# Optimization experiments

Hardware: AMD Instinct MI355X
Metric: run time of the kernel (lower is better)

## Reference

```python
import jax, jax.numpy as jnp
import numpy as np

N, NQ, M, DQ, DK, DV, H = 4, 512, 512, 256, 256, 256, 256


def setup_inputs() -> dict:
    key = jax.random.key(0)
    ks = jax.random.split(key, 6)
    scale_q = 1.0 / np.sqrt(DQ)
    scale_k = 1.0 / np.sqrt(DK)
    scale_v = 1.0 / np.sqrt(H)
    return {
        "query": jax.random.normal(ks[0], (N, NQ, DQ), jnp.float32),
        "key": jax.random.normal(ks[1], (N, M, DK), jnp.float32),
        "value": jax.random.normal(ks[2], (N, M, DV), jnp.float32),
        "W_q": jax.random.normal(ks[3], (DQ, H), jnp.float32) * scale_q,
        "W_k": jax.random.normal(ks[4], (DK, H), jnp.float32) * scale_k,
        "W_v": jax.random.normal(ks[5], (H,), jnp.float32) * scale_v,
    }


def reference(query, key, value, W_q, W_k, W_v):
    # project: (N, n, H) and (N, m, H)
    q = jnp.einsum("bnd,dh->bnh", query, W_q)
    k = jnp.einsum("bmd,dh->bmh", key, W_k)
    # broadcast add -> (N, n, m, H), tanh, project H->1 -> scores (N, n, m)
    scores = jnp.einsum("bnmh,h->bnm", jnp.tanh(q[:, :, None, :] + k[:, None, :, :]), W_v)
    attn = jax.nn.softmax(scores, axis=-1)  # (N, n, m)
    return jnp.einsum("bnm,bmv->bnv", attn, value)
```

## Files before the change

kernel.cpp:

```cpp
#include <hip/hip_runtime.h>
#include <hip/hip_bf16.h>

#define NB 4
#define NQL 512
#define ML 512
#define DDIM 256
#define HDIM 256

static constexpr float TWO_LOG2E = 2.8853900817779268f;
static constexpr float LOG2E     = 1.4426950408889634f;

__global__ __launch_bounds__(256) void proj_kernel(
    const float* __restrict__ q_src, const float* __restrict__ k_src,
    const float* __restrict__ Wq,    const float* __restrict__ Wk,
    float* __restrict__ EqT,         float* __restrict__ EkT)
{
    const int z = blockIdx.z;
    const int b = z & 3;
    const int which = z >> 2;
    const float* __restrict__ src  = which ? k_src : q_src;
    const float* __restrict__ W    = which ? Wk    : Wq;
    float* __restrict__       outT = which ? EkT   : EqT;

    const int l0 = blockIdx.x * 32;
    const int h0 = blockIdx.y * 64;
    const int t  = threadIdx.x;
    const int tx = t & 15;
    const int ty = t >> 4;

    __shared__ float sX[32][36];
    __shared__ float sW[32][68];

    float acc[2][4];
    #pragma unroll
    for (int i = 0; i < 2; i++)
        #pragma unroll
        for (int j = 0; j < 4; j++) acc[i][j] = 0.f;

    const int llA = t >> 3, dgA = t & 7;
    const int ddB = t >> 3, hgB = t & 7;

    for (int d0 = 0; d0 < DDIM; d0 += 32) {
        float4 xv = *(const float4*)&src[(size_t)(b * NQL + l0 + llA) * DDIM + d0 + dgA * 4];
        const float* wrow = &W[(size_t)(d0 + ddB) * HDIM + h0 + hgB * 8];
        float4 wa = ((const float4*)wrow)[0];
        float4 wb = ((const float4*)wrow)[1];
        __syncthreads();
        sX[dgA * 4 + 0][llA] = xv.x;
        sX[dgA * 4 + 1][llA] = xv.y;
        sX[dgA * 4 + 2][llA] = xv.z;
        sX[dgA * 4 + 3][llA] = xv.w;
        *(float4*)&sW[ddB][hgB * 8]     = wa;
        *(float4*)&sW[ddB][hgB * 8 + 4] = wb;
        __syncthreads();
        #pragma unroll
        for (int dd = 0; dd < 32; dd++) {
            float4 w4 = *(const float4*)&sW[dd][tx * 4];
            float2 x2 = *(const float2*)&sX[dd][ty * 2];
            acc[0][0] = fmaf(x2.x, w4.x, acc[0][0]);
            acc[0][1] = fmaf(x2.x, w4.y, acc[0][1]);
            acc[0][2] = fmaf(x2.x, w4.z, acc[0][2]);
            acc[0][3] = fmaf(x2.x, w4.w, acc[0][3]);
            acc[1][0] = fmaf(x2.y, w4.x, acc[1][0]);
            acc[1][1] = fmaf(x2.y, w4.y, acc[1][1]);
            acc[1][2] = fmaf(x2.y, w4.z, acc[1][2]);
            acc[1][3] = fmaf(x2.y, w4.w, acc[1][3]);
        }
    }

    #pragma unroll
    for (int j = 0; j < 4; j++) {
        float2 o;
        o.x = __builtin_amdgcn_exp2f(acc[0][j] * TWO_LOG2E);
        o.y = __builtin_amdgcn_exp2f(acc[1][j] * TWO_LOG2E);
        *(float2*)&outT[(size_t)(b * HDIM + h0 + tx * 4 + j) * NQL + l0 + ty * 2] = o;
    }
}

__global__ __launch_bounds__(256) void scores_kernel(
    const float* __restrict__ EqT, const float* __restrict__ EkT,
    const float* __restrict__ Wv, float* __restrict__ P,
    float* __restrict__ Spart)
{
    const int b  = blockIdx.z;
    const int mt = blockIdx.x;
    const int m0 = mt * 32;
    const int n0 = blockIdx.y * 32;
    const int t  = threadIdx.x;
    const int tx = t & 15;
    const int ty = t >> 4;

    __shared__ float sQ[32][36];
    __shared__ float sK[32][36];
    __shared__ float sWV[32];

    float acc00 = 0.f, acc01 = 0.f, acc10 = 0.f, acc11 = 0.f;
    float swv = 0.f;

    const int hhA = t >> 3, cgA = t & 7;

    for (int h0 = 0; h0 < HDIM; h0 += 32) {
        float4 qv = *(const float4*)&EqT[(size_t)(b * HDIM + h0 + hhA) * NQL + n0 + cgA * 4];
        float4 kv = *(const float4*)&EkT[(size_t)(b * HDIM + h0 + hhA) * ML  + m0 + cgA * 4];
        float wv_ld = (t < 32) ? Wv[h0 + t] : 0.f;
        __syncthreads();
        *(float4*)&sQ[hhA][cgA * 4] = qv;
        *(float4*)&sK[hhA][cgA * 4] = kv;
        if (t < 32) sWV[t] = wv_ld;
        __syncthreads();
        #pragma unroll 8
        for (int hh = 0; hh < 32; hh++) {
            float2 q2 = *(const float2*)&sQ[hh][ty * 2];
            float2 k2 = *(const float2*)&sK[hh][tx * 2];
            float wv = sWV[hh];
            swv += wv;
            const float nw2 = -2.0f * wv;
            float a00 = fmaf(q2.x, k2.x, 1.0f);
            float a01 = fmaf(q2.x, k2.y, 1.0f);
            float a10 = fmaf(q2.y, k2.x, 1.0f);
            float a11 = fmaf(q2.y, k2.y, 1.0f);
            float r0 = __builtin_amdgcn_rcpf(a00 * a01);
            float r1 = __builtin_amdgcn_rcpf(a10 * a11);
            acc00 = fmaf(nw2, r0 * a01, acc00);
            acc01 = fmaf(nw2, r0 * a00, acc01);
            acc10 = fmaf(nw2, r1 * a11, acc10);
            acc11 = fmaf(nw2, r1 * a10, acc11);
        }
    }

    float2 o0, o1;
    o0.x = __builtin_amdgcn_exp2f((swv + acc00) * LOG2E);
    o0.y = __builtin_amdgcn_exp2f((swv + acc01) * LOG2E);
    o1.x = __builtin_amdgcn_exp2f((swv + acc10) * LOG2E);
    o1.y = __builtin_amdgcn_exp2f((swv + acc11) * LOG2E);
    *(float2*)&P[(size_t)(b * NQL + n0 + ty * 2 + 0) * ML + m0 + tx * 2] = o0;
    *(float2*)&P[(size_t)(b * NQL + n0 + ty * 2 + 1) * ML + m0 + tx * 2] = o1;

    float rs0 = o0.x + o0.y;
    float rs1 = o1.x + o1.y;
    #pragma unroll
    for (int off = 1; off < 16; off <<= 1) {
        rs0 += __shfl_xor(rs0, off);
        rs1 += __shfl_xor(rs1, off);
    }
    if (tx == 0) {
        Spart[(size_t)(mt * NB + b) * NQL + n0 + ty * 2 + 0] = rs0;
        Spart[(size_t)(mt * NB + b) * NQL + n0 + ty * 2 + 1] = rs1;
    }
}

__global__ __launch_bounds__(256) void av_kernel(
    const float* __restrict__ A, const float* __restrict__ Spart,
    const float* __restrict__ V, float* __restrict__ O)
{
    const int b  = blockIdx.z;
    const int v0 = blockIdx.x * 64;
    const int n0 = blockIdx.y * 16;
    const int t  = threadIdx.x;
    const int tx = t & 15;
    const int ty = t >> 4;

    __shared__ float sA[32][20];
    __shared__ float sV[32][68];
    __shared__ float sInv[16];

    if (t < 16) {
        float s = 0.f;
        #pragma unroll
        for (int mt = 0; mt < 16; ++mt)
            s += Spart[(size_t)(mt * NB + b) * NQL + n0 + t];
        sInv[t] = 1.0f / s;
    }

    float4 acc = {0.f, 0.f, 0.f, 0.f};

    const int nnA = t >> 4, mgA = t & 15;
    const int mmB = t >> 3, vgB = t & 7;

    for (int m0 = 0; m0 < ML; m0 += 32) {
        float2 av = *(const float2*)&A[(size_t)(b * NQL + n0 + nnA) * ML + m0 + mgA * 2];
        const float* vrow = &V[(size_t)(b * ML + m0 + mmB) * DDIM + v0 + vgB * 8];
        float4 va = ((const float4*)vrow)[0];
        float4 vb = ((const float4*)vrow)[1];
        __syncthreads();
        sA[mgA * 2 + 0][nnA] = av.x;
        sA[mgA * 2 + 1][nnA] = av.y;
        *(float4*)&sV[mmB][vgB * 8]     = va;
        *(float4*)&sV[mmB][vgB * 8 + 4] = vb;
        __syncthreads();
        #pragma unroll
        for (int mm = 0; mm < 32; mm++) {
            float a = sA[mm][ty];
            float4 v4 = *(const float4*)&sV[mm][tx * 4];
            acc.x = fmaf(a, v4.x, acc.x);
            acc.y = fmaf(a, v4.y, acc.y);
            acc.z = fmaf(a, v4.z, acc.z);
            acc.w = fmaf(a, v4.w, acc.w);
        }
    }

    const float inv = sInv[ty];
    float4 o;
    o.x = acc.x * inv;
    o.y = acc.y * inv;
    o.z = acc.z * inv;
    o.w = acc.w * inv;
    *(float4*)&O[(size_t)(b * NQL + n0 + ty) * DDIM + v0 + tx * 4] = o;
}

extern "C" void kernel_launch(void* const* d_in, const int* in_sizes, int n_in,
                              void* d_out, int out_size, void* d_ws, size_t ws_size,
                              hipStream_t stream)
{
    const float* query = (const float*)d_in[0];
    const float* key   = (const float*)d_in[1];
    const float* value = (const float*)d_in[2];
    const float* Wq    = (const float*)d_in[3];
    const float* Wk    = (const float*)d_in[4];
    const float* Wv    = (const float*)d_in[5];
    float* out = (float*)d_out;

    float* EqT   = (float*)d_ws;
    float* EkT   = EqT + (size_t)NB * HDIM * NQL;
    float* P     = EkT + (size_t)NB * HDIM * ML;
    float* Spart = P + (size_t)NB * NQL * ML;

    dim3 gProj(NQL / 32, HDIM / 64, NB * 2);
    proj_kernel<<<gProj, 256, 0, stream>>>(query, key, Wq, Wk, EqT, EkT);

    dim3 gSc(ML / 32, NQL / 32, NB);
    scores_kernel<<<gSc, 256, 0, stream>>>(EqT, EkT, Wv, P, Spart);

    dim3 gAv(DDIM / 64, NQL / 16, NB);
    av_kernel<<<gAv, 256, 0, stream>>>(P, Spart, value, out);
}
```

Measured before the change: 133.6 us.

## Split AV reduction across wavefronts with register prefetch and 4x4 micro-tiles

Restructures the attention-times-value kernel so each of the four wavefronts handles a separate quarter of the m dimension. Each thread now computes a 4x4 register tile instead of 1x4, and the partial sums are combined through shared memory at the end. The next chunk of A and V is loaded into registers while the current chunk is computed, which overlaps global loads with FMAs and cuts the number of loop iterations and barriers. The cost is more shared memory, more registers per thread and an extra reduction step.

```diff
diff --git a/kernel.cpp b/kernel.cpp
--- a/kernel.cpp
+++ b/kernel.cpp
@@ -157,11 +157,14 @@
     const int v0 = blockIdx.x * 64;
     const int n0 = blockIdx.y * 16;
     const int t  = threadIdx.x;
-    const int tx = t & 15;
-    const int ty = t >> 4;
-
-    __shared__ float sA[32][20];
-    __shared__ float sV[32][68];
+    const int lane = t & 63;
+    const int w    = t >> 6;
+    const int tx   = lane & 15;
+    const int tn   = lane >> 4;
+
+    __shared__ float sA[4][32][20];
+    __shared__ float sV[4][32][68];
+    __shared__ float sRed[3][16][64];
     __shared__ float sInv[16];
 
     if (t < 16) {
@@ -172,40 +175,88 @@
         sInv[t] = 1.0f / s;
     }
 
-    float4 acc = {0.f, 0.f, 0.f, 0.f};
-
-    const int nnA = t >> 4, mgA = t & 15;
-    const int mmB = t >> 3, vgB = t & 7;
-
-    for (int m0 = 0; m0 < ML; m0 += 32) {
-        float2 av = *(const float2*)&A[(size_t)(b * NQL + n0 + nnA) * ML + m0 + mgA * 2];
-        const float* vrow = &V[(size_t)(b * ML + m0 + mmB) * DDIM + v0 + vgB * 8];
-        float4 va = ((const float4*)vrow)[0];
-        float4 vb = ((const float4*)vrow)[1];
-        __syncthreads();
-        sA[mgA * 2 + 0][nnA] = av.x;
-        sA[mgA * 2 + 1][nnA] = av.y;
-        *(float4*)&sV[mmB][vgB * 8]     = va;
-        *(float4*)&sV[mmB][vgB * 8 + 4] = vb;
-        __syncthreads();
-        #pragma unroll
-        for (int mm = 0; mm < 32; mm++) {
-            float a = sA[mm][ty];
-            float4 v4 = *(const float4*)&sV[mm][tx * 4];
-            acc.x = fmaf(a, v4.x, acc.x);
-            acc.y = fmaf(a, v4.y, acc.y);
-            acc.z = fmaf(a, v4.z, acc.z);
-            acc.w = fmaf(a, v4.w, acc.w);
-        }
-    }
-
-    const float inv = sInv[ty];
-    float4 o;
-    o.x = acc.x * inv;
-    o.y = acc.y * inv;
-    o.z = acc.z * inv;
-    o.w = acc.w * inv;
-    *(float4*)&O[(size_t)(b * NQL + n0 + ty) * DDIM + v0 + tx * 4] = o;
+    const int nnA = t & 15, wgA = (t >> 4) & 3, mgA = t >> 6;
+    const int vwV = t >> 6, mrV = (t >> 1) & 31, vgV = t & 1;
+
+    const float* abase = &A[(size_t)(b * NQL + n0 + nnA) * ML + wgA * 128 + mgA * 8];
+    const float* vbase = &V[(size_t)(b * ML + vwV * 128 + mrV) * DDIM + v0 + vgV * 32];
+
+    float acc[4][4] = {};
+
+    float4 pa0 = ((const float4*)abase)[0];
+    float4 pa1 = ((const float4*)abase)[1];
+    float4 pv[8];
+    #pragma unroll
+    for (int k = 0; k < 8; ++k) pv[k] = ((const float4*)vbase)[k];
+
+    for (int c = 0; c < 4; ++c) {
+        __syncthreads();
+        sA[wgA][mgA * 8 + 0][nnA] = pa0.x;
+        sA[wgA][mgA * 8 + 1][nnA] = pa0.y;
+        sA[wgA][mgA * 8 + 2][nnA] = pa0.z;
+        sA[wgA][mgA * 8 + 3][nnA] = pa0.w;
+        sA[wgA][mgA * 8 + 4][nnA] = pa1.x;
+        sA[wgA][mgA * 8 + 5][nnA] = pa1.y;
+        sA[wgA][mgA * 8 + 6][nnA] = pa1.z;
+        sA[wgA][mgA * 8 + 7][nnA] = pa1.w;
+        #pragma unroll
+        for (int k = 0; k < 8; ++k)
+            *(float4*)&sV[vwV][mrV][vgV * 32 + k * 4] = pv[k];
+        __syncthreads();
+        if (c < 3) {
+            const float* ap = abase + (c + 1) * 32;
+            pa0 = ((const float4*)ap)[0];
+            pa1 = ((const float4*)ap)[1];
+            const float* vp = vbase + (size_t)(c + 1) * 32 * DDIM;
+            #pragma unroll
+            for (int k = 0; k < 8; ++k) pv[k] = ((const float4*)vp)[k];
+        }
+        #pragma unroll
+        for (int mm = 0; mm < 32; ++mm) {
+            float4 a4 = *(const float4*)&sA[w][mm][tn * 4];
+            float4 v4 = *(const float4*)&sV[w][mm][tx * 4];
+            acc[0][0] = fmaf(a4.x, v4.x, acc[0][0]);
+            acc[0][1] = fmaf(a4.x, v4.y, acc[0][1]);
+            acc[0][2] = fmaf(a4.x, v4.z, acc[0][2]);
+            acc[0][3] = fmaf(a4.x, v4.w, acc[0][3]);
+            acc[1][0] = fmaf(a4.y, v4.x, acc[1][0]);
+            acc[1][1] = fmaf(a4.y, v4.y, acc[1][1]);
+            acc[1][2] = fmaf(a4.y, v4.z, acc[1][2]);
+            acc[1][3] = fmaf(a4.y, v4.w, acc[1][3]);
+            acc[2][0] = fmaf(a4.z, v4.x, acc[2][0]);
+            acc[2][1] = fmaf(a4.z, v4.y, acc[2][1]);
+            acc[2][2] = fmaf(a4.z, v4.z, acc[2][2]);
+            acc[2][3] = fmaf(a4.z, v4.w, acc[2][3]);
+            acc[3][0] = fmaf(a4.w, v4.x, acc[3][0]);
+            acc[3][1] = fmaf(a4.w, v4.y, acc[3][1]);
+            acc[3][2] = fmaf(a4.w, v4.z, acc[3][2]);
+            acc[3][3] = fmaf(a4.w, v4.w, acc[3][3]);
+        }
+    }
+
+    if (w != 0) {
+        #pragma unroll
+        for (int i = 0; i < 4; ++i) {
+            float4 r = {acc[i][0], acc[i][1], acc[i][2], acc[i][3]};
+            *(float4*)&sRed[w - 1][tn * 4 + i][tx * 4] = r;
+        }
+    }
+    __syncthreads();
+    if (w == 0) {
+        #pragma unroll
+        for (int i = 0; i < 4; ++i) {
+            float4 r1 = *(const float4*)&sRed[0][tn * 4 + i][tx * 4];
+            float4 r2 = *(const float4*)&sRed[1][tn * 4 + i][tx * 4];
+            float4 r3 = *(const float4*)&sRed[2][tn * 4 + i][tx * 4];
+            const float inv = sInv[tn * 4 + i];
+            float4 o;
+            o.x = (acc[i][0] + r1.x + r2.x + r3.x) * inv;
+            o.y = (acc[i][1] + r1.y + r2.y + r3.y) * inv;
+            o.z = (acc[i][2] + r1.z + r2.z + r3.z) * inv;
+            o.w = (acc[i][3] + r1.w + r2.w + r3.w) * inv;
+            *(float4*)&O[(size_t)(b * NQL + n0 + tn * 4 + i) * DDIM + v0 + tx * 4] = o;
+        }
+    }
 }
 
 extern "C" void kernel_launch(void* const* d_in, const int* in_sizes, int n_in,
```

Result: slower. 143.5 us (+7.5%).
